# Optimization experiments

Hardware: AMD Instinct MI355X
Metric: run time of the kernel (lower is better)

The kernel has to match this reference:

```python
import jax, jax.numpy as jnp
import numpy as np

B, S, H, M, E = 8, 2048, 2048, 256, 8
Hh = H // 2

def setup_inputs() -> dict:
    key = jax.random.key(0)
    ks = jax.random.split(key, 12)
    s = 0.02
    return {
        "x":   jax.random.normal(ks[0], (B, S, H), dtype=jnp.float32),
        # metacognitive (router) network: H -> M -> M -> E, softmax
        "Wm1": jax.random.normal(ks[1], (H, M), dtype=jnp.float32) * s,
        "bm1": jnp.zeros((M,), dtype=jnp.float32),
        "Wm2": jax.random.normal(ks[2], (M, M), dtype=jnp.float32) * s,
        "bm2": jnp.zeros((M,), dtype=jnp.float32),
        "Wm3": jax.random.normal(ks[3], (M, E), dtype=jnp.float32) * s,
        "bm3": jnp.zeros((E,), dtype=jnp.float32),
        # stacked expert MLPs: Linear(H,H/2)-ReLU-Linear(H/2,H)-Tanh
        "W1":  jax.random.normal(ks[4], (E, H, Hh), dtype=jnp.float32) * s,
        "b1":  jnp.zeros((E, Hh), dtype=jnp.float32),
        "W2":  jax.random.normal(ks[5], (E, Hh, H), dtype=jnp.float32) * s,
        "b2":  jnp.zeros((E, H), dtype=jnp.float32),
        # strategy_effectiveness buffer (init: ones)
        "eff": jnp.ones((E,), dtype=jnp.float32),
    }

def reference(x, Wm1, bm1, Wm2, bm2, Wm3, bm3, W1, b1, W2, b2, eff):
    # --- select_strategy ---
    pooled = x.mean(axis=1)                                   # [B,H]
    h = jax.nn.relu(pooled @ Wm1 + bm1)                       # [B,M]
    h = jax.nn.relu(h @ Wm2 + bm2)                            # [B,M]
    probs = jax.nn.softmax(h @ Wm3 + bm3, axis=-1)            # [B,E]
    w = jax.nn.softmax(probs * eff[None, :], axis=-1)         # [B,E]
    # --- apply_strategies (all experts batched) ---
    he = jax.nn.relu(jnp.einsum('bsh,ehf->bsef', x, W1) + b1) # [B,S,E,Hh]
    ye = jnp.tanh(jnp.einsum('bsef,efh->bseh', he, W2) + b2)  # [B,S,E,H]
    out = jnp.einsum('bseh,be->bsh', ye, w)                   # [B,S,H]
    return out
```

## Files before the change

### kernel.cpp

```cpp
#include <hip/hip_runtime.h>
#include <hip/hip_bf16.h>
#include <cstdint>
#include <cstddef>

#define B_   8
#define S_   2048
#define H_   2048
#define M_   256
#define E_   8
#define HH_  1024
#define BS_  (B_*S_)

typedef _Float16 f16;
typedef _Float16 f16x8 __attribute__((ext_vector_type(8)));
typedef _Float16 f16x4 __attribute__((ext_vector_type(4)));
typedef float    f32x4 __attribute__((ext_vector_type(4)));

#define HSLOT 32768

__device__ __forceinline__ void gl_lds16(const void* g, void* l) {
  __builtin_amdgcn_global_load_lds(
      (const __attribute__((address_space(1))) uint32_t*)g,
      (__attribute__((address_space(3))) uint32_t*)l, 16, 0, 0);
}

__device__ __forceinline__ float fast_tanh(float x) {
  float t = __expf(2.f * x);
  float r = __builtin_amdgcn_rcpf(t + 1.f);
  return __builtin_fmaf(-2.f, r, 1.f);
}

template<int NG, bool SEG, int KB, class F>
__device__ __forceinline__ void kloop(const char* aBlk, const char* bBlk,
                                      char* ldsc, f32x4 (&acc)[8][4], F&& fold) {
  constexpr int NH = NG * 2;
  const int tid = threadIdx.x, ln = tid & 63, wv = tid >> 6;
  const int l15 = ln & 15, kq = ln >> 4;
  const int wm = wv >> 2, wn = wv & 3;

  const char* aPc[2]; const char* bPc[2];
#pragma unroll
  for (int j = 0; j < 2; ++j) {
    int row = (tid >> 2) + j * 128;
    int kqs = (tid & 3) ^ ((row >> 1) & 3);
    aPc[j] = aBlk + (size_t)row * KB + kqs * 16;
    bPc[j] = bBlk + (size_t)row * KB + kqs * 16;
  }
  const int rowA = wm * 128 + l15;
  const int rowB = wn * 64 + l15;
  const int aRd = rowA * 64 + ((kq ^ ((rowA >> 1) & 3)) << 4);
  const int bRd = 16384 + rowB * 64 + ((kq ^ ((rowB >> 1) & 3)) << 4);
  const int dst0 = tid * 16;

  auto stage2 = [&](int Ht, int op) {
    if (Ht >= NH) return;
    char* sb = ldsc + (Ht & 3) * HSLOT;
    size_t oa, ob;
    if constexpr (SEG) {
      size_t kb = (size_t)((Ht & 31) * 64);
      oa = ((size_t)(Ht >> 5) << 25) + kb;
      ob = ((size_t)(Ht >> 5) << 22) + kb;
    } else { oa = ob = (size_t)Ht * 64; }
    if (op == 0) {
      gl_lds16(aPc[0] + oa, sb + dst0);
      gl_lds16(aPc[1] + oa, sb + 8192 + dst0);
    } else {
      gl_lds16(bPc[0] + ob, sb + 16384 + dst0);
      gl_lds16(bPc[1] + ob, sb + 24576 + dst0);
    }
  };

#pragma unroll
  for (int Ht = 0; Ht < 3; ++Ht) { stage2(Ht, 0); stage2(Ht, 1); }
  asm volatile("s_waitcnt vmcnt(8)" ::: "memory");
  __builtin_amdgcn_s_barrier();

#pragma unroll 1
  for (int g = 0; g < NG; ++g) {
#pragma unroll
    for (int kh = 0; kh < 2; ++kh) {
      const int H = g * 2 + kh;
      const char* sb = ldsc + (H & 3) * HSLOT;
      f16x8 bf[4];
#pragma unroll
      for (int mh = 0; mh < 2; ++mh) {
        f16x8 af[4];
        const char* ab = sb + aRd + mh * 4096;
#pragma unroll
        for (int m = 0; m < 4; ++m) af[m] = *(const f16x8*)(ab + m * 1024);
        if (mh == 0) {
          const char* bb = sb + bRd;
#pragma unroll
          for (int n = 0; n < 4; ++n) bf[n] = *(const f16x8*)(bb + n * 1024);
        }
        stage2(H + 3, mh);
        __builtin_amdgcn_s_barrier();
        asm volatile("s_waitcnt lgkmcnt(0)" ::: "memory");
        __builtin_amdgcn_sched_barrier(0);
        __builtin_amdgcn_s_setprio(1);
#pragma unroll
        for (int m = 0; m < 4; ++m)
#pragma unroll
          for (int n = 0; n < 4; ++n)
            acc[mh * 4 + m][n] = __builtin_amdgcn_mfma_f32_16x16x32_f16(
                af[m], bf[n], acc[mh * 4 + m][n], 0, 0, 0);
        __builtin_amdgcn_s_setprio(0);
        __builtin_amdgcn_sched_barrier(0);
        if (mh == 1) {
          if (H < NH - 3)       { asm volatile("s_waitcnt vmcnt(8)" ::: "memory"); }
          else if (H == NH - 3) { asm volatile("s_waitcnt vmcnt(4)" ::: "memory"); }
          else if (H == NH - 2) { asm volatile("s_waitcnt vmcnt(0)" ::: "memory"); }
        }
        __builtin_amdgcn_s_barrier();
      }
    }
    if constexpr (SEG) { if ((g & 15) == 15) fold(g >> 4); }
  }
}

__global__ __launch_bounds__(512, 2) void gemm1_t8(
    const f16* __restrict__ xf, const f16* __restrict__ W1t,
    const float* __restrict__ b1, f16* __restrict__ he) {
  __shared__ alignas(16) char ldsc[4 * HSLOT];
  int id = blockIdx.x;
  int logical = (id & 7) * 256 + (id >> 3);
  int e = logical >> 8, mt = (logical >> 2) & 63, nt = logical & 3;
  int brow = mt * 256, bcol = nt * 256;

  const char* aBlk = (const char*)xf + (size_t)brow * 4096;
  const char* bBlk = (const char*)W1t + ((size_t)e << 22) + (size_t)bcol * 4096;

  f32x4 acc[8][4] = {};
  kloop<32, false, 4096>(aBlk, bBlk, ldsc, acc, [](int) {});

  const int tid = threadIdx.x, ln = tid & 63, wv = tid >> 6;
  const int l15 = ln & 15, kq4 = (ln >> 4) * 4;
  const int wm = wv >> 2, wn = wv & 3;
  f16* C = he + ((size_t)e << 24);
#pragma unroll
  for (int n = 0; n < 4; ++n) {
    int gc = bcol + wn * 64 + n * 16 + l15;
    float bias = b1[e * HH_ + gc];
#pragma unroll
    for (int m = 0; m < 8; ++m) {
      int gr0 = brow + wm * 128 + m * 16 + kq4;
#pragma unroll
      for (int r = 0; r < 4; ++r)
        __builtin_nontemporal_store((f16)fmaxf(acc[m][n][r] + bias, 0.f),
                                    &C[(size_t)(gr0 + r) * HH_ + gc]);
    }
  }
}

__global__ __launch_bounds__(512, 2) void gemm2_t8(
    const f16* __restrict__ he, const f16* __restrict__ W2t,
    const float* __restrict__ b2, const float* __restrict__ wbuf,
    float* __restrict__ out) {
  __shared__ alignas(16) char ldsc[4 * HSLOT];
  __shared__ float biasLDS[E_][256];
  __shared__ float wLDS[E_];
  int id = blockIdx.x;
  int logical = (id & 7) * 64 + (id >> 3);
  int mt = logical >> 3, nt = logical & 7;
  int brow = mt * 256, bcol = nt * 256;
  int bb = brow >> 11;

  const int tid = threadIdx.x, ln = tid & 63, wv = tid >> 6;
  const int l15 = ln & 15, kq4 = (ln >> 4) * 4;
  const int wm = wv >> 2, wn = wv & 3;

  {
    int i = tid;
#pragma unroll
    for (int rep = 0; rep < 4; ++rep, i += 512)
      biasLDS[i >> 8][i & 255] = b2[(size_t)(i >> 8) * H_ + bcol + (i & 255)];
    if (tid < E_) wLDS[tid] = wbuf[bb * E_ + tid];
  }
  __syncthreads();

  const char* aBlk = (const char*)he + (size_t)brow * 2048;
  const char* bBlk = (const char*)W2t + (size_t)bcol * 2048;

  f32x4 acc[8][4] = {};
  f16x4 tot[8][4] = {};

  auto fold = [&](int e) {
    float we = wLDS[e];
#pragma unroll
    for (int n = 0; n < 4; ++n) {
      float bias = biasLDS[e][wn * 64 + n * 16 + l15];
#pragma unroll
      for (int m = 0; m < 8; ++m) {
#pragma unroll
        for (int r = 0; r < 4; ++r) {
          tot[m][n][r] += (f16)(we * fast_tanh(acc[m][n][r] + bias));
          acc[m][n][r] = 0.f;
        }
      }
    }
  };

  kloop<128, true, 2048>(aBlk, bBlk, ldsc, acc, fold);

#pragma unroll
  for (int n = 0; n < 4; ++n) {
    int gc = bcol + wn * 64 + n * 16 + l15;
#pragma unroll
    for (int m = 0; m < 8; ++m) {
      int gr0 = brow + wm * 128 + m * 16 + kq4;
#pragma unroll
      for (int r = 0; r < 4; ++r)
        __builtin_nontemporal_store((float)tot[m][n][r],
                                    &out[(size_t)(gr0 + r) * H_ + gc]);
    }
  }
}

__global__ void convert_x_pool(const float* __restrict__ x, f16* __restrict__ xf,
                               float* __restrict__ partial) {
  int h  = blockIdx.x * 256 + threadIdx.x;
  int sc = blockIdx.y;
  int b  = blockIdx.z;
  size_t base = ((size_t)b * S_ + sc * 64) * H_ + h;
  float sum = 0.f;
#pragma unroll 4
  for (int i = 0; i < 64; ++i) {
    float v = x[base + (size_t)i * H_];
    sum += v;
    xf[base + (size_t)i * H_] = (f16)v;
  }
  partial[((size_t)b * H_ + h) * 32 + sc] = sum;
}

__global__ void router_kernel(const float* __restrict__ partial,
                              const float* __restrict__ Wm1, const float* __restrict__ bm1,
                              const float* __restrict__ Wm2, const float* __restrict__ bm2,
                              const float* __restrict__ Wm3, const float* __restrict__ bm3,
                              const float* __restrict__ eff, float* __restrict__ wout) {
  __shared__ float pl[H_];
  __shared__ float h1[M_];
  __shared__ float h2[M_];
  __shared__ float lg[E_];
  int b = blockIdx.x;
  int t = threadIdx.x;

  for (int i = t; i < H_; i += 256) {
    float s = 0.f;
    const float* p = partial + ((size_t)b * H_ + i) * 32;
#pragma unroll
    for (int c = 0; c < 32; ++c) s += p[c];
    pl[i] = s * (1.0f / S_);
  }
  __syncthreads();

  float s = bm1[t];
  for (int k = 0; k < H_; ++k) s += pl[k] * Wm1[(size_t)k * M_ + t];
  h1[t] = fmaxf(s, 0.f);
  __syncthreads();

  s = bm2[t];
  for (int k = 0; k < M_; ++k) s += h1[k] * Wm2[k * M_ + t];
  h2[t] = fmaxf(s, 0.f);
  __syncthreads();

  if (t < E_) {
    float l = bm3[t];
    for (int k = 0; k < M_; ++k) l += h2[k] * Wm3[k * E_ + t];
    lg[t] = l;
  }
  __syncthreads();

  if (t == 0) {
    float p[E_], q[E_];
    float mx = -1e30f;
    for (int e = 0; e < E_; ++e) mx = fmaxf(mx, lg[e]);
    float den = 0.f;
    for (int e = 0; e < E_; ++e) { p[e] = __expf(lg[e] - mx); den += p[e]; }
    float inv = 1.f / den;
    for (int e = 0; e < E_; ++e) q[e] = p[e] * inv * eff[e];
    mx = -1e30f;
    for (int e = 0; e < E_; ++e) mx = fmaxf(mx, q[e]);
    den = 0.f;
    for (int e = 0; e < E_; ++e) { q[e] = __expf(q[e] - mx); den += q[e]; }
    inv = 1.f / den;
    for (int e = 0; e < E_; ++e) wout[b * E_ + e] = q[e] * inv;
  }
}

__global__ void transpose_cvt(const float* __restrict__ in, f16* __restrict__ out,
                              int R, int C) {
  __shared__ f16 tile[32][33];
  int e  = blockIdx.z;
  int c0 = blockIdx.x * 32, r0 = blockIdx.y * 32;
  int tx = threadIdx.x & 31, ty = threadIdx.x >> 5;
  const float* inp = in + (size_t)e * R * C;
  f16* outp = out + (size_t)e * R * C;
#pragma unroll
  for (int i = 0; i < 4; ++i) {
    int r = r0 + ty + i * 8;
    tile[ty + i * 8][tx] = (f16)inp[(size_t)r * C + c0 + tx];
  }
  __syncthreads();
#pragma unroll
  for (int i = 0; i < 4; ++i) {
    int c = c0 + ty + i * 8;
    outp[(size_t)c * R + r0 + tx] = tile[tx][ty + i * 8];
  }
}

extern "C" void kernel_launch(void* const* d_in, const int* in_sizes, int n_in,
                              void* d_out, int out_size, void* d_ws, size_t ws_size,
                              hipStream_t stream) {
  const float* x   = (const float*)d_in[0];
  const float* Wm1 = (const float*)d_in[1];
  const float* bm1 = (const float*)d_in[2];
  const float* Wm2 = (const float*)d_in[3];
  const float* bm2 = (const float*)d_in[4];
  const float* Wm3 = (const float*)d_in[5];
  const float* bm3 = (const float*)d_in[6];
  const float* W1  = (const float*)d_in[7];
  const float* b1  = (const float*)d_in[8];
  const float* W2  = (const float*)d_in[9];
  const float* b2  = (const float*)d_in[10];
  const float* eff = (const float*)d_in[11];
  float* out = (float*)d_out;

  char* ws = (char*)d_ws;
  size_t off = 0;
  auto take = [&](size_t bytes) { void* p = ws + off; off += (bytes + 255) & ~(size_t)255; return p; };

  f16*   xf      = (f16*)  take((size_t)BS_ * H_ * 2);
  f16*   W1t     = (f16*)  take((size_t)E_ * HH_ * H_ * 2);
  f16*   W2t     = (f16*)  take((size_t)E_ * H_ * HH_ * 2);
  float* partial = (float*)take((size_t)B_ * H_ * 32 * 4);
  float* wbuf    = (float*)take(1024);
  f16*   he      = (f16*)  take((size_t)E_ * BS_ * HH_ * 2);

  convert_x_pool<<<dim3(H_ / 256, S_ / 64, B_), 256, 0, stream>>>(x, xf, partial);
  router_kernel<<<B_, 256, 0, stream>>>(partial, Wm1, bm1, Wm2, bm2, Wm3, bm3, eff, wbuf);
  transpose_cvt<<<dim3(HH_ / 32, H_ / 32, E_), 256, 0, stream>>>(W1, W1t, H_, HH_);
  transpose_cvt<<<dim3(H_ / 32, HH_ / 32, E_), 256, 0, stream>>>(W2, W2t, HH_, H_);

  gemm1_t8<<<2048, 512, 0, stream>>>(xf, W1t, b1, he);
  gemm2_t8<<<512, 512, 0, stream>>>(he, W2t, b2, wbuf, out);
}
```

Baseline: 1.424 ms.

## Load GEMM1 B operand directly from global into registers, stage only A in LDS

The generic kloop in the first expert GEMM is replaced by a custom main loop. Only the x tile is staged through LDS, in a 4-deep ring of 16KB slots with an XOR-swizzled layout. Each wave reads its W1 fragments straight from global memory into registers, double-buffered one k-step ahead. This halves LDS traffic and footprint per block, but makes the MFMA stream depend on global-load latency for B. The output store also switches from nontemporal to a regular store.

```diff
diff --git a/kernel.cpp b/kernel.cpp
--- a/kernel.cpp
+++ b/kernel.cpp
@@ -118,24 +118,91 @@
   }
 }
 
-__global__ __launch_bounds__(512, 2) void gemm1_t8(
+#define REGION1(H, bfU, bfL)                                                   \
+  {                                                                            \
+    const char* sb = ldsc + ((H) & 3) * 16384;                                 \
+    f16x8 af0[4], af1[4];                                                      \
+    _Pragma("unroll")                                                          \
+    for (int m = 0; m < 4; ++m) af0[m] = *(const f16x8*)(sb + aRd + m * 1024); \
+    _Pragma("unroll")                                                          \
+    for (int m = 0; m < 4; ++m) af1[m] = *(const f16x8*)(sb + aRd + 4096 + m * 1024); \
+    int Hn = (H) + 1 < 64 ? (H) + 1 : 63;                                      \
+    _Pragma("unroll")                                                          \
+    for (int n = 0; n < 4; ++n) bfL[n] = *(const f16x8*)(bP[n] + (size_t)Hn * 64); \
+    stageA((H) + 3);                                                           \
+    __builtin_amdgcn_s_setprio(1);                                             \
+    _Pragma("unroll")                                                          \
+    for (int m = 0; m < 4; ++m)                                                \
+      _Pragma("unroll")                                                        \
+      for (int n = 0; n < 4; ++n)                                              \
+        acc[m][n] = __builtin_amdgcn_mfma_f32_16x16x32_f16(af0[m], bfU[n], acc[m][n], 0, 0, 0); \
+    _Pragma("unroll")                                                          \
+    for (int m = 0; m < 4; ++m)                                                \
+      _Pragma("unroll")                                                        \
+      for (int n = 0; n < 4; ++n)                                              \
+        acc[4 + m][n] = __builtin_amdgcn_mfma_f32_16x16x32_f16(af1[m], bfU[n], acc[4 + m][n], 0, 0, 0); \
+    __builtin_amdgcn_s_setprio(0);                                             \
+    __builtin_amdgcn_s_barrier();                                              \
+  }
+
+__global__ __launch_bounds__(512, 2) void gemm1_v11(
     const f16* __restrict__ xf, const f16* __restrict__ W1t,
     const float* __restrict__ b1, f16* __restrict__ he) {
-  __shared__ alignas(16) char ldsc[4 * HSLOT];
+  __shared__ alignas(16) char ldsc[4 * 16384];
   int id = blockIdx.x;
   int logical = (id & 7) * 256 + (id >> 3);
   int e = logical >> 8, mt = (logical >> 2) & 63, nt = logical & 3;
   int brow = mt * 256, bcol = nt * 256;
 
+  const int tid = threadIdx.x, ln = tid & 63, wv = tid >> 6;
+  const int l15 = ln & 15, kq = ln >> 4;
+  const int wm = wv >> 2, wn = wv & 3;
+
   const char* aBlk = (const char*)xf + (size_t)brow * 4096;
-  const char* bBlk = (const char*)W1t + ((size_t)e << 22) + (size_t)bcol * 4096;
+  const char* bBase = (const char*)W1t + ((size_t)e << 22) + (size_t)bcol * 4096;
+
+  const char* aPc[2];
+#pragma unroll
+  for (int j = 0; j < 2; ++j) {
+    int row = (tid >> 2) + j * 128;
+    int kqs = (tid & 3) ^ ((row >> 1) & 3);
+    aPc[j] = aBlk + (size_t)row * 4096 + kqs * 16;
+  }
+  const int rowA = wm * 128 + l15;
+  const int aRd = rowA * 64 + ((kq ^ ((rowA >> 1) & 3)) << 4);
+  const int dst0 = tid * 16;
+
+  const char* bP[4];
+#pragma unroll
+  for (int n = 0; n < 4; ++n) {
+    int row = wn * 64 + n * 16 + l15;
+    bP[n] = bBase + (size_t)row * 4096 + kq * 16;
+  }
+
+  auto stageA = [&](int Ht) {
+    if (Ht >= 64) return;
+    char* sb = ldsc + (Ht & 3) * 16384;
+    size_t ko = (size_t)Ht * 64;
+    gl_lds16(aPc[0] + ko, sb + dst0);
+    gl_lds16(aPc[1] + ko, sb + 8192 + dst0);
+  };
 
   f32x4 acc[8][4] = {};
-  kloop<32, false, 4096>(aBlk, bBlk, ldsc, acc, [](int) {});
-
-  const int tid = threadIdx.x, ln = tid & 63, wv = tid >> 6;
-  const int l15 = ln & 15, kq4 = (ln >> 4) * 4;
-  const int wm = wv >> 2, wn = wv & 3;
+
+  stageA(0); stageA(1); stageA(2);
+  asm volatile("s_waitcnt vmcnt(4)" ::: "memory");
+  __builtin_amdgcn_s_barrier();
+  f16x8 bfA[4], bfB[4];
+#pragma unroll
+  for (int n = 0; n < 4; ++n) bfA[n] = *(const f16x8*)(bP[n]);
+
+#pragma unroll 1
+  for (int g = 0; g < 32; ++g) {
+    REGION1(2 * g,     bfA, bfB);
+    REGION1(2 * g + 1, bfB, bfA);
+  }
+
+  const int kq4 = kq * 4;
   f16* C = he + ((size_t)e << 24);
 #pragma unroll
   for (int n = 0; n < 4; ++n) {
@@ -146,8 +213,7 @@
       int gr0 = brow + wm * 128 + m * 16 + kq4;
 #pragma unroll
       for (int r = 0; r < 4; ++r)
-        __builtin_nontemporal_store((f16)fmaxf(acc[m][n][r] + bias, 0.f),
-                                    &C[(size_t)(gr0 + r) * HH_ + gc]);
+        C[(size_t)(gr0 + r) * HH_ + gc] = (f16)fmaxf(acc[m][n][r] + bias, 0.f);
     }
   }
 }
@@ -341,6 +407,6 @@
   transpose_cvt<<<dim3(HH_ / 32, H_ / 32, E_), 256, 0, stream>>>(W1, W1t, H_, HH_);
   transpose_cvt<<<dim3(H_ / 32, HH_ / 32, E_), 256, 0, stream>>>(W2, W2t, HH_, H_);
 
-  gemm1_t8<<<2048, 512, 0, stream>>>(xf, W1t, b1, he);
+  gemm1_v11<<<2048, 512, 0, stream>>>(xf, W1t, b1, he);
   gemm2_t8<<<512, 512, 0, stream>>>(he, W2t, b2, wbuf, out);
 }
```

Result: slower. 1.699 ms (+19.3%).
